# Optimization experiments

Hardware: AMD Instinct MI355X
Metric: run time of the kernel (lower is better)

The kernel has to match this reference:

```python
import jax, jax.numpy as jnp
import numpy as np
import math

N = 100000
D = 128      # input_dim
H = 4        # heads
DK = 32      # d_k
DV = D // H  # d_v = 32


def setup_inputs() -> dict:
    key = jax.random.key(0)
    k1, k2, k3, k4, k5 = jax.random.split(key, 5)
    x = jax.random.normal(k1, (N, D), dtype=jnp.float32)
    neighbor_index = jax.random.randint(k2, (N, 4), 0, N, dtype=jnp.int64)
    w_q = jax.random.normal(k3, (H, D, DK), dtype=jnp.float32) * 0.05
    w_k = jax.random.normal(k4, (H, 5, D, DK), dtype=jnp.float32) * 0.05
    w_v = jax.random.normal(k5, (H, 5, D, DV), dtype=jnp.float32) * 0.05
    return {"x": x, "neighbor_index": neighbor_index, "w_q": w_q, "w_k": w_k, "w_v": w_v}


def reference(x, neighbor_index, w_q, w_k, w_v):
    n = x.shape[0]
    d_k = w_q.shape[-1]
    # gather 4 neighbors, prepend self node -> (N, 5, D)
    x_neighbors = jnp.concatenate([x[:, None, :], x[neighbor_index]], axis=1)
    Q = jnp.einsum('nd,hdk->hnk', x, w_q)                 # (H, N, DK)
    K = jnp.einsum('nrd,hrdk->hnrk', x_neighbors, w_k)    # (H, N, 5, DK)
    V = jnp.einsum('nrd,hrdv->hnrv', x_neighbors, w_v)    # (H, N, 5, DV)
    A = jnp.einsum('hnk,hnrk->hnr', Q, K) / math.sqrt(d_k)
    # NOTE: original torch code applies softmax over dim=1, which is the NODE
    # dimension (not the neighbor dimension r). Replicated faithfully.
    A = jax.nn.softmax(A, axis=1)
    Z = jnp.einsum('hnr,hnrv->hnv', A, V)                 # (H, N, DV)
    return Z.transpose(1, 0, 2).reshape(n, -1)            # (N, H*DV)
```

## Files before the change

### kernel.cpp

```cpp
#include <hip/hip_runtime.h>


#define N_NODES 100000
#define D 128
#define H 4
#define R 5
#define NPB 64
#define THREADS 256
#define NBLOCKS ((N_NODES + NPB - 1) / NPB)

typedef _Float16 half_t;
typedef __attribute__((ext_vector_type(8))) _Float16 f16x8;
typedef __attribute__((ext_vector_type(4))) float f32x4;

typedef const __attribute__((address_space(1))) unsigned int* gp_t;
typedef __attribute__((address_space(3))) unsigned int* lp_t;

__device__ __forceinline__ void async_copy16(const void* g, void* l) {
    __builtin_amdgcn_global_load_lds((gp_t)g, (lp_t)l, 16, 0, 0);
}

template<int V> struct ic { static constexpr int value = V; };

__global__ void prep(const float* __restrict__ x,
                     const float* __restrict__ wq, const float* __restrict__ wk,
                     const float* __restrict__ wv,
                     half_t* __restrict__ xh, half_t* __restrict__ wph)
{
    const int bid = blockIdx.x;
    const int t = threadIdx.x;
    if (bid < 44) {
        const float* src = (bid < 4) ? (wq + bid * 4096)
                         : (bid < 24) ? (wk + (bid - 4) * 4096)
                                      : (wv + (bid - 24) * 4096);
#pragma unroll
        for (int i = 0; i < 16; ++i) {
            int p = t * 16 + i;
            int j = p & 7, ln = (p >> 3) & 63, f = p >> 9;
            int kt = f & 3, mt = f >> 2;
            int d = kt * 32 + (ln >> 4) * 8 + j;
            int ko = mt * 16 + (ln & 15);
            wph[bid * 4096 + p] = (half_t)src[d * 32 + ko];
        }
    } else {
        const int total = N_NODES * D / 8;
        const int nb = gridDim.x - 44;
        for (int i = (bid - 44) * THREADS + t; i < total; i += nb * THREADS) {
            const float4* s = (const float4*)x + (size_t)i * 2;
            float4 a = s[0], b = s[1];
            f16x8 h8 = {(half_t)a.x, (half_t)a.y, (half_t)a.z, (half_t)a.w,
                        (half_t)b.x, (half_t)b.y, (half_t)b.z, (half_t)b.w};
            *((f16x8*)xh + i) = h8;
        }
    }
}

template<int SLOT>
__device__ __forceinline__ void stage_slot(const half_t* __restrict__ xh,
                                           const int (&rows)[4], const int4 (&nb4)[4],
                                           int base, char* buf, int lane)
{
    const int rr = lane >> 4;
    const int c = lane & 15;
#pragma unroll
    for (int i = 0; i < 4; ++i) {
        int row = rows[i];
        int src;
        if constexpr (SLOT == 0) {
            int node = base + row;
            src = (node >= N_NODES) ? (N_NODES - 1) : node;
        } else if constexpr (SLOT == 1) src = nb4[i].x;
        else if constexpr (SLOT == 2) src = nb4[i].y;
        else if constexpr (SLOT == 3) src = nb4[i].z;
        else                          src = nb4[i].w;
        const char* g = (const char*)xh + (size_t)src * 256 + ((c ^ (row & 7)) << 4);
        async_copy16(g, buf + (row - rr) * 256);
    }
}

__device__ __forceinline__ void load_af(int mid, const half_t* __restrict__ wph,
                                        int lane, f16x8 (&af)[8])
{
#pragma unroll
    for (int kt = 0; kt < 4; ++kt) {
        af[kt * 2]     = *(const f16x8*)(wph + ((mid * 8 + kt) * 64 + lane) * 8);
        af[kt * 2 + 1] = *(const f16x8*)(wph + ((mid * 8 + 4 + kt) * 64 + lane) * 8);
    }
}

__device__ __forceinline__ void proj_mfma(const f16x8 (&af)[8], const half_t* tile,
                                          int lane, f32x4 (&acc)[2][4])
{
    const int l15 = lane & 15, q = lane >> 4;
#pragma unroll
    for (int mt = 0; mt < 2; ++mt)
#pragma unroll
        for (int nt = 0; nt < 4; ++nt)
            acc[mt][nt] = (f32x4){0.f, 0.f, 0.f, 0.f};
#pragma unroll
    for (int kt = 0; kt < 4; ++kt) {
#pragma unroll
        for (int nt = 0; nt < 4; ++nt) {
            int row = nt * 16 + l15;
            int sq = (kt * 4 + q) ^ (row & 7);
            f16x8 b = *(const f16x8*)(tile + row * 128 + sq * 8);
            acc[0][nt] = __builtin_amdgcn_mfma_f32_16x16x32_f16(af[kt * 2], b, acc[0][nt], 0, 0, 0);
            acc[1][nt] = __builtin_amdgcn_mfma_f32_16x16x32_f16(af[kt * 2 + 1], b, acc[1][nt], 0, 0, 0);
        }
    }
}

__global__ __launch_bounds__(THREADS, 3)
void knot_logits(const half_t* __restrict__ xh, const int* __restrict__ nbr,
                 const half_t* __restrict__ wph,
                 half_t* __restrict__ eh, float* __restrict__ sums_p)
{
    __shared__ __align__(16) char bufA[NPB * 256];
    __shared__ __align__(16) char bufB[NPB * 256];
    const int base = blockIdx.x * NPB;
    const int lane = threadIdx.x & 63;
    const int h = __builtin_amdgcn_readfirstlane((int)(threadIdx.x >> 6));
    const int l15 = lane & 15, rr = lane >> 4;

    int rows[4]; int4 nb4[4];
#pragma unroll
    for (int i = 0; i < 4; ++i) {
        rows[i] = h * 16 + i * 4 + rr;
        int node = base + rows[i];
        if (node >= N_NODES) node = N_NODES - 1;
        nb4[i] = ((const int4*)nbr)[node];
    }

    stage_slot<0>(xh, rows, nb4, base, bufA, lane);
    stage_slot<1>(xh, rows, nb4, base, bufB, lane);
    __syncthreads();

    f16x8 af[8];
    f32x4 qf[2][4], kf[2][4];
    load_af(h, wph, lane, af);
    proj_mfma(af, (const half_t*)bufA, lane, qf);

    auto slot = [&](auto rc) {
        constexpr int r = decltype(rc)::value;
        const half_t* cur = (const half_t*)((r & 1) ? bufB : bufA);
        char* nxt = ((r + 1) & 1) ? bufB : bufA;
        load_af(4 + h * 5 + r, wph, lane, af);
        if constexpr (r >= 1 && r <= 3) {
            __builtin_amdgcn_sched_barrier(0);
            stage_slot<r + 1>(xh, rows, nb4, base, nxt, lane);
        }
        proj_mfma(af, cur, lane, kf);

        float esum = 0.f;
#pragma unroll
        for (int nt = 0; nt < 4; ++nt) {
            float p = 0.f;
#pragma unroll
            for (int mt = 0; mt < 2; ++mt)
#pragma unroll
                for (int j = 0; j < 4; ++j)
                    p += qf[mt][nt][j] * kf[mt][nt][j];
            p += __shfl_xor(p, 16, 64);
            p += __shfl_xor(p, 32, 64);
            int node = base + nt * 16 + l15;
            float e = (node < N_NODES) ? __expf(p * 0.17677669529663688f) : 0.f;
            if (rr == 0 && node < N_NODES)
                eh[(size_t)(h * 5 + r) * N_NODES + node] = (half_t)e;
            esum += e;
        }
        esum += __shfl_xor(esum, 1, 64);
        esum += __shfl_xor(esum, 2, 64);
        esum += __shfl_xor(esum, 4, 64);
        esum += __shfl_xor(esum, 8, 64);
        if (lane == 0)
            atomicAdd(&sums_p[(h * 5 + r) * 64 + (blockIdx.x & 63)], esum);
        __syncthreads();
    };
    slot(ic<0>{}); slot(ic<1>{}); slot(ic<2>{}); slot(ic<3>{}); slot(ic<4>{});
}

#define VS 67
__global__ __launch_bounds__(THREADS, 3)
void knot_out(const half_t* __restrict__ xh, const int* __restrict__ nbr,
              const half_t* __restrict__ wph, const half_t* __restrict__ eh,
              const float* __restrict__ sums_p, float* __restrict__ out)
{
    __shared__ __align__(16) char bufA[NPB * 256];
    __shared__ __align__(16) char bufB[NPB * 256];
    __shared__ float sums_s[20];
    const int base = blockIdx.x * NPB;
    const int lane = threadIdx.x & 63;
    const int h = __builtin_amdgcn_readfirstlane((int)(threadIdx.x >> 6));
    const int l15 = lane & 15, rr = lane >> 4, q = rr;

#pragma unroll
    for (int i = 0; i < 5; ++i) {
        int hr = h * 5 + i;
        float v = sums_p[hr * 64 + lane];
        v += __shfl_xor(v, 1, 64);  v += __shfl_xor(v, 2, 64);
        v += __shfl_xor(v, 4, 64);  v += __shfl_xor(v, 8, 64);
        v += __shfl_xor(v, 16, 64); v += __shfl_xor(v, 32, 64);
        if (lane == 0) sums_s[hr] = v;
    }

    int rows[4]; int4 nb4[4];
#pragma unroll
    for (int i = 0; i < 4; ++i) {
        rows[i] = h * 16 + i * 4 + rr;
        int node = base + rows[i];
        if (node >= N_NODES) node = N_NODES - 1;
        nb4[i] = ((const int4*)nbr)[node];
    }

    stage_slot<0>(xh, rows, nb4, base, bufA, lane);
    stage_slot<1>(xh, rows, nb4, base, bufB, lane);
    __syncthreads();

    float inv[5];
#pragma unroll
    for (int r = 0; r < 5; ++r) inv[r] = 1.0f / sums_s[h * 5 + r];

    f16x8 af[8];
    f32x4 z[2][4], vf[2][4];
#pragma unroll
    for (int mt = 0; mt < 2; ++mt)
#pragma unroll
        for (int nt = 0; nt < 4; ++nt)
            z[mt][nt] = (f32x4){0.f, 0.f, 0.f, 0.f};

    auto slot = [&](auto rc) {
        constexpr int r = decltype(rc)::value;
        const half_t* cur = (const half_t*)((r & 1) ? bufB : bufA);
        char* nxt = ((r + 1) & 1) ? bufB : bufA;
        load_af(24 + h * 5 + r, wph, lane, af);
        float ev[4];
#pragma unroll
        for (int nt = 0; nt < 4; ++nt) {
            int node = base + nt * 16 + l15;
            if (node >= N_NODES) node = N_NODES - 1;
            ev[nt] = (float)eh[(size_t)(h * 5 + r) * N_NODES + node];
        }
        if constexpr (r >= 1 && r <= 3) {
            __builtin_amdgcn_sched_barrier(0);
            stage_slot<r + 1>(xh, rows, nb4, base, nxt, lane);
        }
        proj_mfma(af, cur, lane, vf);
#pragma unroll
        for (int nt = 0; nt < 4; ++nt) {
            float w = ev[nt] * inv[r];
#pragma unroll
            for (int mt = 0; mt < 2; ++mt)
#pragma unroll
                for (int j = 0; j < 4; ++j)
                    z[mt][nt][j] += w * vf[mt][nt][j];
        }
        __syncthreads();
    };
    slot(ic<0>{}); slot(ic<1>{}); slot(ic<2>{}); slot(ic<3>{}); slot(ic<4>{});

#pragma unroll 1
    for (int pass = 0; pass < 2; ++pass) {
        if (pass) __syncthreads();
        if ((h >> 1) == pass) {
            float* ztp = (float*)((h & 1) ? bufB : bufA);
#pragma unroll
            for (int mt = 0; mt < 2; ++mt)
#pragma unroll
                for (int nt = 0; nt < 4; ++nt)
#pragma unroll
                    for (int j = 0; j < 4; ++j) {
                        int v = mt * 16 + q * 4 + j;
                        ztp[v * VS + nt * 16 + l15] = z[mt][nt][j];
                    }
        }
        __syncthreads();
        const int row = threadIdx.x >> 2;
        const int c = threadIdx.x & 3;
        if (base + row < N_NODES) {
            float* dst = out + (size_t)(base + row) * D + pass * 64 + c * 16;
#pragma unroll
            for (int i4 = 0; i4 < 4; ++i4) {
                float4 v4;
#pragma unroll
                for (int e = 0; e < 4; ++e) {
                    int col = c * 16 + i4 * 4 + e;
                    const float* ztp = (const float*)((col & 32) ? bufB : bufA);
                    ((float*)&v4)[e] = ztp[(col & 31) * VS + row];
                }
                *(float4*)(dst + i4 * 4) = v4;
            }
        }
    }
}

extern "C" void kernel_launch(void* const* d_in, const int* in_sizes, int n_in,
                              void* d_out, int out_size, void* d_ws, size_t ws_size,
                              hipStream_t stream)
{
    const float* x   = (const float*)d_in[0];
    const int*   nbr = (const int*)d_in[1];
    const float* w_q = (const float*)d_in[2];
    const float* w_k = (const float*)d_in[3];
    const float* w_v = (const float*)d_in[4];
    float* out = (float*)d_out;

    float*  sums_p = (float*)d_ws;
    half_t* eh     = (half_t*)((char*)d_ws + 8192);
    half_t* wph    = (half_t*)((char*)d_ws + 4194304);
    half_t* xh     = (half_t*)((char*)d_ws + 4718592);

    hipMemsetAsync(d_ws, 0, 5120, stream);
    prep<<<44 + 2048, THREADS, 0, stream>>>(x, w_q, w_k, w_v, xh, wph);
    knot_logits<<<NBLOCKS, THREADS, 0, stream>>>(xh, nbr, wph, eh, sums_p);
    knot_out<<<NBLOCKS, THREADS, 0, stream>>>(xh, nbr, wph, eh, sums_p, out);
}
```

Baseline: 205.6 us.

## Load gathered rows straight from global into MFMA operands, drop LDS staging

Removes the async global-to-LDS double-buffered staging of gathered neighbor rows. Each wave now loads its MFMA B operands directly from the fp16 x copy in global memory, using per-lane neighbor indices that are prefetched one slot ahead. The per-slot block barriers go away, LDS drops to just the output transpose buffer, and launch bounds rise to 4 blocks per SM. The separate memset is folded into the prep kernel. In exchange, every head's wave re-reads the same gathered rows from global/L2 instead of sharing one LDS copy, and there is no explicit overlap of the next slot's loads.

```diff
diff --git a/kernel.cpp b/kernel.cpp
--- a/kernel.cpp
+++ b/kernel.cpp
@@ -13,19 +13,11 @@
 typedef __attribute__((ext_vector_type(8))) _Float16 f16x8;
 typedef __attribute__((ext_vector_type(4))) float f32x4;
 
-typedef const __attribute__((address_space(1))) unsigned int* gp_t;
-typedef __attribute__((address_space(3))) unsigned int* lp_t;
-
-__device__ __forceinline__ void async_copy16(const void* g, void* l) {
-    __builtin_amdgcn_global_load_lds((gp_t)g, (lp_t)l, 16, 0, 0);
-}
-
-template<int V> struct ic { static constexpr int value = V; };
-
 __global__ void prep(const float* __restrict__ x,
                      const float* __restrict__ wq, const float* __restrict__ wk,
                      const float* __restrict__ wv,
-                     half_t* __restrict__ xh, half_t* __restrict__ wph)
+                     half_t* __restrict__ xh, half_t* __restrict__ wph,
+                     float* __restrict__ sums_p)
 {
     const int bid = blockIdx.x;
     const int t = threadIdx.x;
@@ -43,6 +35,9 @@
             wph[bid * 4096 + p] = (half_t)src[d * 32 + ko];
         }
     } else {
+        if (bid == 44) {
+            for (int i = t; i < 1280; i += THREADS) sums_p[i] = 0.f;
+        }
         const int total = N_NODES * D / 8;
         const int nb = gridDim.x - 44;
         for (int i = (bid - 44) * THREADS + t; i < total; i += nb * THREADS) {
@@ -55,29 +50,6 @@
     }
 }
 
-template<int SLOT>
-__device__ __forceinline__ void stage_slot(const half_t* __restrict__ xh,
-                                           const int (&rows)[4], const int4 (&nb4)[4],
-                                           int base, char* buf, int lane)
-{
-    const int rr = lane >> 4;
-    const int c = lane & 15;
-#pragma unroll
-    for (int i = 0; i < 4; ++i) {
-        int row = rows[i];
-        int src;
-        if constexpr (SLOT == 0) {
-            int node = base + row;
-            src = (node >= N_NODES) ? (N_NODES - 1) : node;
-        } else if constexpr (SLOT == 1) src = nb4[i].x;
-        else if constexpr (SLOT == 2) src = nb4[i].y;
-        else if constexpr (SLOT == 3) src = nb4[i].z;
-        else                          src = nb4[i].w;
-        const char* g = (const char*)xh + (size_t)src * 256 + ((c ^ (row & 7)) << 4);
-        async_copy16(g, buf + (row - rr) * 256);
-    }
-}
-
 __device__ __forceinline__ void load_af(int mid, const half_t* __restrict__ wph,
                                         int lane, f16x8 (&af)[8])
 {
@@ -88,68 +60,71 @@
     }
 }
 
-__device__ __forceinline__ void proj_mfma(const f16x8 (&af)[8], const half_t* tile,
-                                          int lane, f32x4 (&acc)[2][4])
-{
-    const int l15 = lane & 15, q = lane >> 4;
+__device__ __forceinline__ void proj_g(const f16x8 (&af)[8],
+                                       const half_t* __restrict__ xh,
+                                       const int (&src)[4], int q,
+                                       f32x4 (&acc)[2][4])
+{
 #pragma unroll
     for (int mt = 0; mt < 2; ++mt)
 #pragma unroll
         for (int nt = 0; nt < 4; ++nt)
             acc[mt][nt] = (f32x4){0.f, 0.f, 0.f, 0.f};
 #pragma unroll
-    for (int kt = 0; kt < 4; ++kt) {
-#pragma unroll
-        for (int nt = 0; nt < 4; ++nt) {
-            int row = nt * 16 + l15;
-            int sq = (kt * 4 + q) ^ (row & 7);
-            f16x8 b = *(const f16x8*)(tile + row * 128 + sq * 8);
+    for (int nt = 0; nt < 4; ++nt) {
+        const half_t* p = xh + (size_t)src[nt] * 128 + q * 8;
+#pragma unroll
+        for (int kt = 0; kt < 4; ++kt) {
+            f16x8 b = *(const f16x8*)(p + kt * 32);
             acc[0][nt] = __builtin_amdgcn_mfma_f32_16x16x32_f16(af[kt * 2], b, acc[0][nt], 0, 0, 0);
             acc[1][nt] = __builtin_amdgcn_mfma_f32_16x16x32_f16(af[kt * 2 + 1], b, acc[1][nt], 0, 0, 0);
         }
     }
 }
 
-__global__ __launch_bounds__(THREADS, 3)
+__global__ __launch_bounds__(THREADS, 4)
 void knot_logits(const half_t* __restrict__ xh, const int* __restrict__ nbr,
                  const half_t* __restrict__ wph,
                  half_t* __restrict__ eh, float* __restrict__ sums_p)
 {
-    __shared__ __align__(16) char bufA[NPB * 256];
-    __shared__ __align__(16) char bufB[NPB * 256];
     const int base = blockIdx.x * NPB;
     const int lane = threadIdx.x & 63;
     const int h = __builtin_amdgcn_readfirstlane((int)(threadIdx.x >> 6));
-    const int l15 = lane & 15, rr = lane >> 4;
-
-    int rows[4]; int4 nb4[4];
-#pragma unroll
-    for (int i = 0; i < 4; ++i) {
-        rows[i] = h * 16 + i * 4 + rr;
-        int node = base + rows[i];
-        if (node >= N_NODES) node = N_NODES - 1;
-        nb4[i] = ((const int4*)nbr)[node];
-    }
-
-    stage_slot<0>(xh, rows, nb4, base, bufA, lane);
-    stage_slot<1>(xh, rows, nb4, base, bufB, lane);
-    __syncthreads();
+    const int l15 = lane & 15, q = lane >> 4;
+
+    int self[4];
+#pragma unroll
+    for (int nt = 0; nt < 4; ++nt) {
+        int node = base + nt * 16 + l15;
+        self[nt] = (node >= N_NODES) ? (N_NODES - 1) : node;
+    }
 
     f16x8 af[8];
     f32x4 qf[2][4], kf[2][4];
     load_af(h, wph, lane, af);
-    proj_mfma(af, (const half_t*)bufA, lane, qf);
-
-    auto slot = [&](auto rc) {
-        constexpr int r = decltype(rc)::value;
-        const half_t* cur = (const half_t*)((r & 1) ? bufB : bufA);
-        char* nxt = ((r + 1) & 1) ? bufB : bufA;
+    proj_g(af, xh, self, q, qf);
+
+    int src_cur[4], src_nxt[4];
+#pragma unroll
+    for (int nt = 0; nt < 4; ++nt) {
+        src_cur[nt] = self[nt];
+        src_nxt[nt] = nbr[self[nt] * 4 + 0];
+    }
+
+#pragma unroll 1
+    for (int r = 0; r < R; ++r) {
         load_af(4 + h * 5 + r, wph, lane, af);
-        if constexpr (r >= 1 && r <= 3) {
-            __builtin_amdgcn_sched_barrier(0);
-            stage_slot<r + 1>(xh, rows, nb4, base, nxt, lane);
-        }
-        proj_mfma(af, cur, lane, kf);
+        proj_g(af, xh, src_cur, q, kf);
+
+        if (r < R - 1) {
+#pragma unroll
+            for (int nt = 0; nt < 4; ++nt) src_cur[nt] = src_nxt[nt];
+            if (r < R - 2) {
+#pragma unroll
+                for (int nt = 0; nt < 4; ++nt)
+                    src_nxt[nt] = nbr[self[nt] * 4 + (r + 1)];
+            }
+        }
 
         float esum = 0.f;
 #pragma unroll
@@ -164,7 +139,7 @@
             p += __shfl_xor(p, 32, 64);
             int node = base + nt * 16 + l15;
             float e = (node < N_NODES) ? __expf(p * 0.17677669529663688f) : 0.f;
-            if (rr == 0 && node < N_NODES)
+            if (q == 0 && node < N_NODES)
                 eh[(size_t)(h * 5 + r) * N_NODES + node] = (half_t)e;
             esum += e;
         }
@@ -174,24 +149,21 @@
         esum += __shfl_xor(esum, 8, 64);
         if (lane == 0)
             atomicAdd(&sums_p[(h * 5 + r) * 64 + (blockIdx.x & 63)], esum);
-        __syncthreads();
-    };
-    slot(ic<0>{}); slot(ic<1>{}); slot(ic<2>{}); slot(ic<3>{}); slot(ic<4>{});
+    }
 }
 
 #define VS 67
-__global__ __launch_bounds__(THREADS, 3)
+__global__ __launch_bounds__(THREADS, 4)
 void knot_out(const half_t* __restrict__ xh, const int* __restrict__ nbr,
               const half_t* __restrict__ wph, const half_t* __restrict__ eh,
               const float* __restrict__ sums_p, float* __restrict__ out)
 {
-    __shared__ __align__(16) char bufA[NPB * 256];
-    __shared__ __align__(16) char bufB[NPB * 256];
+    __shared__ float zt[2 * 32 * VS];
     __shared__ float sums_s[20];
     const int base = blockIdx.x * NPB;
     const int lane = threadIdx.x & 63;
     const int h = __builtin_amdgcn_readfirstlane((int)(threadIdx.x >> 6));
-    const int l15 = lane & 15, rr = lane >> 4, q = rr;
+    const int l15 = lane & 15, q = lane >> 4;
 
 #pragma unroll
     for (int i = 0; i < 5; ++i) {
@@ -202,23 +174,14 @@
         v += __shfl_xor(v, 16, 64); v += __shfl_xor(v, 32, 64);
         if (lane == 0) sums_s[hr] = v;
     }
-
-    int rows[4]; int4 nb4[4];
-#pragma unroll
-    for (int i = 0; i < 4; ++i) {
-        rows[i] = h * 16 + i * 4 + rr;
-        int node = base + rows[i];
-        if (node >= N_NODES) node = N_NODES - 1;
-        nb4[i] = ((const int4*)nbr)[node];
-    }
-
-    stage_slot<0>(xh, rows, nb4, base, bufA, lane);
-    stage_slot<1>(xh, rows, nb4, base, bufB, lane);
     __syncthreads();
 
-    float inv[5];
-#pragma unroll
-    for (int r = 0; r < 5; ++r) inv[r] = 1.0f / sums_s[h * 5 + r];
+    int self[4];
+#pragma unroll
+    for (int nt = 0; nt < 4; ++nt) {
+        int node = base + nt * 16 + l15;
+        self[nt] = (node >= N_NODES) ? (N_NODES - 1) : node;
+    }
 
     f16x8 af[8];
     f32x4 z[2][4], vf[2][4];
@@ -228,41 +191,48 @@
         for (int nt = 0; nt < 4; ++nt)
             z[mt][nt] = (f32x4){0.f, 0.f, 0.f, 0.f};
 
-    auto slot = [&](auto rc) {
-        constexpr int r = decltype(rc)::value;
-        const half_t* cur = (const half_t*)((r & 1) ? bufB : bufA);
-        char* nxt = ((r + 1) & 1) ? bufB : bufA;
+    int src_cur[4], src_nxt[4];
+#pragma unroll
+    for (int nt = 0; nt < 4; ++nt) {
+        src_cur[nt] = self[nt];
+        src_nxt[nt] = nbr[self[nt] * 4 + 0];
+    }
+
+#pragma unroll 1
+    for (int r = 0; r < R; ++r) {
         load_af(24 + h * 5 + r, wph, lane, af);
         float ev[4];
 #pragma unroll
+        for (int nt = 0; nt < 4; ++nt)
+            ev[nt] = (float)eh[(size_t)(h * 5 + r) * N_NODES + self[nt]];
+        proj_g(af, xh, src_cur, q, vf);
+
+        if (r < R - 1) {
+#pragma unroll
+            for (int nt = 0; nt < 4; ++nt) src_cur[nt] = src_nxt[nt];
+            if (r < R - 2) {
+#pragma unroll
+                for (int nt = 0; nt < 4; ++nt)
+                    src_nxt[nt] = nbr[self[nt] * 4 + (r + 1)];
+            }
+        }
+
+        float inv = 1.0f / sums_s[h * 5 + r];
+#pragma unroll
         for (int nt = 0; nt < 4; ++nt) {
-            int node = base + nt * 16 + l15;
-            if (node >= N_NODES) node = N_NODES - 1;
-            ev[nt] = (float)eh[(size_t)(h * 5 + r) * N_NODES + node];
-        }
-        if constexpr (r >= 1 && r <= 3) {
-            __builtin_amdgcn_sched_barrier(0);
-            stage_slot<r + 1>(xh, rows, nb4, base, nxt, lane);
-        }
-        proj_mfma(af, cur, lane, vf);
-#pragma unroll
-        for (int nt = 0; nt < 4; ++nt) {
-            float w = ev[nt] * inv[r];
+            float w = ev[nt] * inv;
 #pragma unroll
             for (int mt = 0; mt < 2; ++mt)
 #pragma unroll
                 for (int j = 0; j < 4; ++j)
                     z[mt][nt][j] += w * vf[mt][nt][j];
         }
-        __syncthreads();
-    };
-    slot(ic<0>{}); slot(ic<1>{}); slot(ic<2>{}); slot(ic<3>{}); slot(ic<4>{});
+    }
 
 #pragma unroll 1
     for (int pass = 0; pass < 2; ++pass) {
-        if (pass) __syncthreads();
+        __syncthreads();
         if ((h >> 1) == pass) {
-            float* ztp = (float*)((h & 1) ? bufB : bufA);
 #pragma unroll
             for (int mt = 0; mt < 2; ++mt)
 #pragma unroll
@@ -270,7 +240,7 @@
 #pragma unroll
                     for (int j = 0; j < 4; ++j) {
                         int v = mt * 16 + q * 4 + j;
-                        ztp[v * VS + nt * 16 + l15] = z[mt][nt][j];
+                        zt[(h & 1) * 32 * VS + v * VS + nt * 16 + l15] = z[mt][nt][j];
                     }
         }
         __syncthreads();
@@ -284,8 +254,7 @@
 #pragma unroll
                 for (int e = 0; e < 4; ++e) {
                     int col = c * 16 + i4 * 4 + e;
-                    const float* ztp = (const float*)((col & 32) ? bufB : bufA);
-                    ((float*)&v4)[e] = ztp[(col & 31) * VS + row];
+                    ((float*)&v4)[e] = zt[(col >> 5) * 32 * VS + (col & 31) * VS + row];
                 }
                 *(float4*)(dst + i4 * 4) = v4;
             }
@@ -309,8 +278,7 @@
     half_t* wph    = (half_t*)((char*)d_ws + 4194304);
     half_t* xh     = (half_t*)((char*)d_ws + 4718592);
 
-    hipMemsetAsync(d_ws, 0, 5120, stream);
-    prep<<<44 + 2048, THREADS, 0, stream>>>(x, w_q, w_k, w_v, xh, wph);
+    prep<<<44 + 2048, THREADS, 0, stream>>>(x, w_q, w_k, w_v, xh, wph, sums_p);
     knot_logits<<<NBLOCKS, THREADS, 0, stream>>>(xh, nbr, wph, eh, sums_p);
     knot_out<<<NBLOCKS, THREADS, 0, stream>>>(xh, nbr, wph, eh, sums_p, out);
 }
```

Result: slower. 301.5 us (+46.6%).

## Triple-buffer neighbor staging with manual vmcnt waits and fold memset into prep

Applied to the files above, without the earlier changes.

Both main kernels go from double to triple LDS buffering of the gathered neighbor rows. Full __syncthreads after each slot are replaced by explicit s_waitcnt vmcnt plus s_barrier, so loads for later slots can stay in flight across the projection MFMAs. The logits kernel keeps the exp values in registers and defers the eh stores and atomics to the end, and the output kernel prefetches all eh values up front. The hipMemsetAsync is removed by zeroing the sums in prep, saving one launch. LDS per block rises to 48KB, which may limit occupancy, and the hand-tuned vmcnt counts are fragile if the compiler reorders loads.

```diff
diff --git a/kernel.cpp b/kernel.cpp
--- a/kernel.cpp
+++ b/kernel.cpp
@@ -10,22 +10,25 @@
 #define NBLOCKS ((N_NODES + NPB - 1) / NPB)
 
 typedef _Float16 half_t;
+typedef __attribute__((ext_vector_type(2))) _Float16 f16x2;
 typedef __attribute__((ext_vector_type(8))) _Float16 f16x8;
 typedef __attribute__((ext_vector_type(4))) float f32x4;
 
 typedef const __attribute__((address_space(1))) unsigned int* gp_t;
 typedef __attribute__((address_space(3))) unsigned int* lp_t;
 
+#define WAITVM(N) asm volatile("s_waitcnt vmcnt(" #N ")" ::: "memory")
+#define BARRIER() asm volatile("s_barrier" ::: "memory")
+
 __device__ __forceinline__ void async_copy16(const void* g, void* l) {
     __builtin_amdgcn_global_load_lds((gp_t)g, (lp_t)l, 16, 0, 0);
 }
-
-template<int V> struct ic { static constexpr int value = V; };
 
 __global__ void prep(const float* __restrict__ x,
                      const float* __restrict__ wq, const float* __restrict__ wk,
                      const float* __restrict__ wv,
-                     half_t* __restrict__ xh, half_t* __restrict__ wph)
+                     half_t* __restrict__ xh, half_t* __restrict__ wph,
+                     float* __restrict__ sums_p)
 {
     const int bid = blockIdx.x;
     const int t = threadIdx.x;
@@ -43,6 +46,9 @@
             wph[bid * 4096 + p] = (half_t)src[d * 32 + ko];
         }
     } else {
+        if (bid == 44) {
+            for (int i = t; i < 1280; i += THREADS) sums_p[i] = 0.f;
+        }
         const int total = N_NODES * D / 8;
         const int nb = gridDim.x - 44;
         for (int i = (bid - 44) * THREADS + t; i < total; i += nb * THREADS) {
@@ -110,13 +116,37 @@
     }
 }
 
+#define LOGIT_MATH(r)                                                         \
+    {   float es_ = 0.f;                                                      \
+        _Pragma("unroll")                                                     \
+        for (int nt = 0; nt < 4; ++nt) {                                      \
+            float p = 0.f;                                                    \
+            _Pragma("unroll")                                                 \
+            for (int mt = 0; mt < 2; ++mt)                                    \
+                _Pragma("unroll")                                             \
+                for (int j = 0; j < 4; ++j)                                   \
+                    p += qf[mt][nt][j] * kf[mt][nt][j];                       \
+            p += __shfl_xor(p, 16, 64);                                       \
+            p += __shfl_xor(p, 32, 64);                                       \
+            int node = base + nt * 16 + l15;                                  \
+            float e = (node < N_NODES) ? __expf(p * 0.17677669529663688f) : 0.f; \
+            epk[r][nt >> 1][nt & 1] = (half_t)e;                              \
+            es_ += e;                                                         \
+        }                                                                     \
+        es_ += __shfl_xor(es_, 1, 64); es_ += __shfl_xor(es_, 2, 64);         \
+        es_ += __shfl_xor(es_, 4, 64); es_ += __shfl_xor(es_, 8, 64);         \
+        esum[r] = es_;                                                        \
+    }
+
 __global__ __launch_bounds__(THREADS, 3)
 void knot_logits(const half_t* __restrict__ xh, const int* __restrict__ nbr,
                  const half_t* __restrict__ wph,
                  half_t* __restrict__ eh, float* __restrict__ sums_p)
 {
-    __shared__ __align__(16) char bufA[NPB * 256];
-    __shared__ __align__(16) char bufB[NPB * 256];
+    __shared__ __align__(16) char smem[3 * 16384];
+    char* buf0 = smem;
+    char* buf1 = smem + 16384;
+    char* buf2 = smem + 32768;
     const int base = blockIdx.x * NPB;
     const int lane = threadIdx.x & 63;
     const int h = __builtin_amdgcn_readfirstlane((int)(threadIdx.x >> 6));
@@ -130,63 +160,88 @@
         if (node >= N_NODES) node = N_NODES - 1;
         nb4[i] = ((const int4*)nbr)[node];
     }
-
-    stage_slot<0>(xh, rows, nb4, base, bufA, lane);
-    stage_slot<1>(xh, rows, nb4, base, bufB, lane);
-    __syncthreads();
+    stage_slot<0>(xh, rows, nb4, base, buf0, lane);
+    stage_slot<1>(xh, rows, nb4, base, buf1, lane);
 
     f16x8 af[8];
     f32x4 qf[2][4], kf[2][4];
+    f16x2 epk[5][2];
+    float esum[5];
+
     load_af(h, wph, lane, af);
-    proj_mfma(af, (const half_t*)bufA, lane, qf);
-
-    auto slot = [&](auto rc) {
-        constexpr int r = decltype(rc)::value;
-        const half_t* cur = (const half_t*)((r & 1) ? bufB : bufA);
-        char* nxt = ((r + 1) & 1) ? bufB : bufA;
-        load_af(4 + h * 5 + r, wph, lane, af);
-        if constexpr (r >= 1 && r <= 3) {
-            __builtin_amdgcn_sched_barrier(0);
-            stage_slot<r + 1>(xh, rows, nb4, base, nxt, lane);
-        }
-        proj_mfma(af, cur, lane, kf);
-
-        float esum = 0.f;
-#pragma unroll
-        for (int nt = 0; nt < 4; ++nt) {
-            float p = 0.f;
-#pragma unroll
-            for (int mt = 0; mt < 2; ++mt)
-#pragma unroll
-                for (int j = 0; j < 4; ++j)
-                    p += qf[mt][nt][j] * kf[mt][nt][j];
-            p += __shfl_xor(p, 16, 64);
-            p += __shfl_xor(p, 32, 64);
-            int node = base + nt * 16 + l15;
-            float e = (node < N_NODES) ? __expf(p * 0.17677669529663688f) : 0.f;
-            if (rr == 0 && node < N_NODES)
-                eh[(size_t)(h * 5 + r) * N_NODES + node] = (half_t)e;
-            esum += e;
-        }
-        esum += __shfl_xor(esum, 1, 64);
-        esum += __shfl_xor(esum, 2, 64);
-        esum += __shfl_xor(esum, 4, 64);
-        esum += __shfl_xor(esum, 8, 64);
+    WAITVM(8);
+    BARRIER();
+    stage_slot<2>(xh, rows, nb4, base, buf2, lane);
+    proj_mfma(af, (const half_t*)buf0, lane, qf);
+
+    load_af(4 + h * 5 + 0, wph, lane, af);
+    WAITVM(12);
+    BARRIER();
+    proj_mfma(af, (const half_t*)buf0, lane, kf);
+    LOGIT_MATH(0)
+
+    load_af(4 + h * 5 + 1, wph, lane, af);
+    WAITVM(12);
+    BARRIER();
+    stage_slot<3>(xh, rows, nb4, base, buf0, lane);
+    proj_mfma(af, (const half_t*)buf1, lane, kf);
+    LOGIT_MATH(1)
+
+    load_af(4 + h * 5 + 2, wph, lane, af);
+    WAITVM(12);
+    BARRIER();
+    stage_slot<4>(xh, rows, nb4, base, buf1, lane);
+    proj_mfma(af, (const half_t*)buf2, lane, kf);
+    LOGIT_MATH(2)
+
+    load_af(4 + h * 5 + 3, wph, lane, af);
+    WAITVM(12);
+    BARRIER();
+    proj_mfma(af, (const half_t*)buf0, lane, kf);
+    LOGIT_MATH(3)
+
+    load_af(4 + h * 5 + 4, wph, lane, af);
+    WAITVM(8);
+    BARRIER();
+    proj_mfma(af, (const half_t*)buf1, lane, kf);
+    LOGIT_MATH(4)
+
+#pragma unroll
+    for (int r = 0; r < 5; ++r) {
+        if (rr == 0) {
+#pragma unroll
+            for (int nt = 0; nt < 4; ++nt) {
+                int node = base + nt * 16 + l15;
+                if (node < N_NODES)
+                    eh[(size_t)(h * 5 + r) * N_NODES + node] = epk[r][nt >> 1][nt & 1];
+            }
+        }
         if (lane == 0)
-            atomicAdd(&sums_p[(h * 5 + r) * 64 + (blockIdx.x & 63)], esum);
-        __syncthreads();
-    };
-    slot(ic<0>{}); slot(ic<1>{}); slot(ic<2>{}); slot(ic<3>{}); slot(ic<4>{});
+            atomicAdd(&sums_p[(h * 5 + r) * 64 + (blockIdx.x & 63)], esum[r]);
+    }
 }
 
 #define VS 67
+#define VACCUM(r)                                                             \
+    _Pragma("unroll")                                                         \
+    for (int nt = 0; nt < 4; ++nt) {                                          \
+        float w = ev[r][nt] * inv[r];                                         \
+        _Pragma("unroll")                                                     \
+        for (int mt = 0; mt < 2; ++mt)                                        \
+            _Pragma("unroll")                                                 \
+            for (int j = 0; j < 4; ++j)                                       \
+                z[mt][nt][j] += w * vf[mt][nt][j];                            \
+    }
+
 __global__ __launch_bounds__(THREADS, 3)
 void knot_out(const half_t* __restrict__ xh, const int* __restrict__ nbr,
               const half_t* __restrict__ wph, const half_t* __restrict__ eh,
               const float* __restrict__ sums_p, float* __restrict__ out)
 {
-    __shared__ __align__(16) char bufA[NPB * 256];
-    __shared__ __align__(16) char bufB[NPB * 256];
+    __shared__ __align__(16) char smem[3 * 16384];
+    char* buf0 = smem;
+    char* buf1 = smem + 16384;
+    char* buf2 = smem + 32768;
     __shared__ float sums_s[20];
     const int base = blockIdx.x * NPB;
     const int lane = threadIdx.x & 63;
@@ -202,6 +257,24 @@
         v += __shfl_xor(v, 16, 64); v += __shfl_xor(v, 32, 64);
         if (lane == 0) sums_s[hr] = v;
     }
+    __syncthreads();
+
+    float inv[5];
+#pragma unroll
+    for (int r = 0; r < 5; ++r) inv[r] = 1.0f / sums_s[h * 5 + r];
+
+    int self[4];
+#pragma unroll
+    for (int nt = 0; nt < 4; ++nt) {
+        int node = base + nt * 16 + l15;
+        self[nt] = (node >= N_NODES) ? (N_NODES - 1) : node;
+    }
+    float ev[5][4];
+#pragma unroll
+    for (int r = 0; r < 5; ++r)
+#pragma unroll
+        for (int nt = 0; nt < 4; ++nt)
+            ev[r][nt] = (float)eh[(size_t)(h * 5 + r) * N_NODES + self[nt]];
 
     int rows[4]; int4 nb4[4];
 #pragma unroll
@@ -211,14 +284,8 @@
         if (node >= N_NODES) node = N_NODES - 1;
         nb4[i] = ((const int4*)nbr)[node];
     }
-
-    stage_slot<0>(xh, rows, nb4, base, bufA, lane);
-    stage_slot<1>(xh, rows, nb4, base, bufB, lane);
-    __syncthreads();
-
-    float inv[5];
-#pragma unroll
-    for (int r = 0; r < 5; ++r) inv[r] = 1.0f / sums_s[h * 5 + r];
+    stage_slot<0>(xh, rows, nb4, base, buf0, lane);
+    stage_slot<1>(xh, rows, nb4, base, buf1, lane);
 
     f16x8 af[8];
     f32x4 z[2][4], vf[2][4];
@@ -228,41 +295,44 @@
         for (int nt = 0; nt < 4; ++nt)
             z[mt][nt] = (f32x4){0.f, 0.f, 0.f, 0.f};
 
-    auto slot = [&](auto rc) {
-        constexpr int r = decltype(rc)::value;
-        const half_t* cur = (const half_t*)((r & 1) ? bufB : bufA);
-        char* nxt = ((r + 1) & 1) ? bufB : bufA;
-        load_af(24 + h * 5 + r, wph, lane, af);
-        float ev[4];
-#pragma unroll
-        for (int nt = 0; nt < 4; ++nt) {
-            int node = base + nt * 16 + l15;
-            if (node >= N_NODES) node = N_NODES - 1;
-            ev[nt] = (float)eh[(size_t)(h * 5 + r) * N_NODES + node];
-        }
-        if constexpr (r >= 1 && r <= 3) {
-            __builtin_amdgcn_sched_barrier(0);
-            stage_slot<r + 1>(xh, rows, nb4, base, nxt, lane);
-        }
-        proj_mfma(af, cur, lane, vf);
-#pragma unroll
-        for (int nt = 0; nt < 4; ++nt) {
-            float w = ev[nt] * inv[r];
-#pragma unroll
-            for (int mt = 0; mt < 2; ++mt)
-#pragma unroll
-                for (int j = 0; j < 4; ++j)
-                    z[mt][nt][j] += w * vf[mt][nt][j];
-        }
-        __syncthreads();
-    };
-    slot(ic<0>{}); slot(ic<1>{}); slot(ic<2>{}); slot(ic<3>{}); slot(ic<4>{});
-
+    load_af(24 + h * 5 + 0, wph, lane, af);
+    WAITVM(8);
+    BARRIER();
+    stage_slot<2>(xh, rows, nb4, base, buf2, lane);
+    proj_mfma(af, (const half_t*)buf0, lane, vf);
+    VACCUM(0)
+
+    load_af(24 + h * 5 + 1, wph, lane, af);
+    WAITVM(12);
+    BARRIER();
+    stage_slot<3>(xh, rows, nb4, base, buf0, lane);
+    proj_mfma(af, (const half_t*)buf1, lane, vf);
+    VACCUM(1)
+
+    load_af(24 + h * 5 + 2, wph, lane, af);
+    WAITVM(12);
+    BARRIER();
+    stage_slot<4>(xh, rows, nb4, base, buf1, lane);
+    proj_mfma(af, (const half_t*)buf2, lane, vf);
+    VACCUM(2)
+
+    load_af(24 + h * 5 + 3, wph, lane, af);
+    WAITVM(12);
+    BARRIER();
+    proj_mfma(af, (const half_t*)buf0, lane, vf);
+    VACCUM(3)
+
+    load_af(24 + h * 5 + 4, wph, lane, af);
+    WAITVM(8);
+    BARRIER();
+    proj_mfma(af, (const half_t*)buf1, lane, vf);
+    VACCUM(4)
+
+    float* zt = (float*)smem;
 #pragma unroll 1
     for (int pass = 0; pass < 2; ++pass) {
-        if (pass) __syncthreads();
+        __syncthreads();
         if ((h >> 1) == pass) {
-            float* ztp = (float*)((h & 1) ? bufB : bufA);
 #pragma unroll
             for (int mt = 0; mt < 2; ++mt)
 #pragma unroll
@@ -270,7 +340,7 @@
 #pragma unroll
                     for (int j = 0; j < 4; ++j) {
                         int v = mt * 16 + q * 4 + j;
-                        ztp[v * VS + nt * 16 + l15] = z[mt][nt][j];
+                        zt[(h & 1) * 32 * VS + v * VS + nt * 16 + l15] = z[mt][nt][j];
                     }
         }
         __syncthreads();
@@ -284,8 +354,7 @@
 #pragma unroll
                 for (int e = 0; e < 4; ++e) {
                     int col = c * 16 + i4 * 4 + e;
-                    const float* ztp = (const float*)((col & 32) ? bufB : bufA);
-                    ((float*)&v4)[e] = ztp[(col & 31) * VS + row];
+                    ((float*)&v4)[e] = zt[(col >> 5) * 32 * VS + (col & 31) * VS + row];
                 }
                 *(float4*)(dst + i4 * 4) = v4;
             }
@@ -309,8 +378,7 @@
     half_t* wph    = (half_t*)((char*)d_ws + 4194304);
     half_t* xh     = (half_t*)((char*)d_ws + 4718592);
 
-    hipMemsetAsync(d_ws, 0, 5120, stream);
-    prep<<<44 + 2048, THREADS, 0, stream>>>(x, w_q, w_k, w_v, xh, wph);
+    prep<<<44 + 2048, THREADS, 0, stream>>>(x, w_q, w_k, w_v, xh, wph, sums_p);
     knot_logits<<<NBLOCKS, THREADS, 0, stream>>>(xh, nbr, wph, eh, sums_p);
     knot_out<<<NBLOCKS, THREADS, 0, stream>>>(xh, nbr, wph, eh, sums_p, out);
 }
```

New measurement: 190.8 us. 7.2% less time.
